# Kernel optimization log

Hardware: AMD Instinct MI355X
Metric: run time of the kernel (lower is better)

Reference implementation:

```python
import jax, jax.numpy as jnp
import numpy as np

SHIFT = 7  # shift_size; pad = 3


def _gn(x, w, b, eps=1e-5):
    # GroupNorm(1, C): normalize over (C,H,W) per sample, affine per channel
    m = jnp.mean(x, axis=(1, 2, 3), keepdims=True)
    v = jnp.var(x, axis=(1, 2, 3), keepdims=True)
    return (x - m) * jax.lax.rsqrt(v + eps) * w[None, :, None, None] + b[None, :, None, None]


def _conv1x1(x, w, b):
    return jnp.einsum('bchw,oc->bohw', x, w) + b[None, :, None, None]


def _gelu(x):
    return jax.nn.gelu(x, approximate=False)


def _shift_h(x, size):
    # CUDA kernel semantics: g = c // ceil(C/size); s = -(g - size//2);
    # out[n,c,h,w] = x[n,c,h+s,w] if in-bounds else 0  (dim=2)
    B, C, H, W = x.shape
    pad = size // 2
    group = -(-C // size)  # ceil
    s = pad - (jnp.arange(C) // group)              # [C], values in [-pad, pad]
    xp = jnp.pad(x, ((0, 0), (0, 0), (pad, pad), (0, 0)))
    idx = jnp.arange(H)[None, :] + s[:, None] + pad  # [C,H], in [0, H+2p-1]
    c = jnp.arange(C)[:, None]
    return xp[:, c, idx, :]


def _shift_w(x, size):
    return _shift_h(x.swapaxes(2, 3), size).swapaxes(2, 3)


def _axial_shift(x, c1w, c1b, n1w, n1b, c21w, c21b, c22w, c22b, n2w, n2b, c3w, c3b):
    x = _gelu(_gn(_conv1x1(x, c1w, c1b), n1w, n1b))
    x_lr = _shift_w(x, SHIFT)
    x_td = _shift_h(x, SHIFT)
    x_lr = _gelu(_conv1x1(x_lr, c21w, c21b))
    x_td = _gelu(_conv1x1(x_td, c22w, c22b))
    x = _gn(x_lr + x_td, n2w, n2b)
    return _conv1x1(x, c3w, c3b)


def setup_inputs() -> dict:
    B, C, H, W = 16, 256, 56, 56
    HID = 4 * C
    key = jax.random.key(0)
    ks = jax.random.split(key, 8)
    wscale = 0.05
    inp = {
        'x': jax.random.normal(ks[0], (B, C, H, W), jnp.float32),
        'n1_w': jnp.ones((C,), jnp.float32), 'n1_b': jnp.zeros((C,), jnp.float32),
        'as_c1_w': jax.random.normal(ks[1], (C, C), jnp.float32) * wscale,
        'as_c1_b': jnp.zeros((C,), jnp.float32),
        'as_n1_w': jnp.ones((C,), jnp.float32), 'as_n1_b': jnp.zeros((C,), jnp.float32),
        'as_c21_w': jax.random.normal(ks[2], (C, C), jnp.float32) * wscale,
        'as_c21_b': jnp.zeros((C,), jnp.float32),
        'as_c22_w': jax.random.normal(ks[3], (C, C), jnp.float32) * wscale,
        'as_c22_b': jnp.zeros((C,), jnp.float32),
        'as_n2_w': jnp.ones((C,), jnp.float32), 'as_n2_b': jnp.zeros((C,), jnp.float32),
        'as_c3_w': jax.random.normal(ks[4], (C, C), jnp.float32) * wscale,
        'as_c3_b': jnp.zeros((C,), jnp.float32),
        'n2_w': jnp.ones((C,), jnp.float32), 'n2_b': jnp.zeros((C,), jnp.float32),
        'fc1_w': jax.random.normal(ks[5], (HID, C), jnp.float32) * wscale,
        'fc1_b': jnp.zeros((HID,), jnp.float32),
        'fc2_w': jax.random.normal(ks[6], (C, HID), jnp.float32) * wscale,
        'fc2_b': jnp.zeros((C,), jnp.float32),
    }
    return inp


def reference(x, n1_w, n1_b, as_c1_w, as_c1_b, as_n1_w, as_n1_b,
              as_c21_w, as_c21_b, as_c22_w, as_c22_b, as_n2_w, as_n2_b,
              as_c3_w, as_c3_b, n2_w, n2_b, fc1_w, fc1_b, fc2_w, fc2_b):
    # AxialShiftedBlock: x = x + AxialShift(norm1(x)); x = x + Mlp(norm2(x))
    h = _gn(x, n1_w, n1_b)
    h = _axial_shift(h, as_c1_w, as_c1_b, as_n1_w, as_n1_b,
                     as_c21_w, as_c21_b, as_c22_w, as_c22_b,
                     as_n2_w, as_n2_b, as_c3_w, as_c3_b)
    x = x + h
    h = _gn(x, n2_w, n2_b)
    h = _gelu(_conv1x1(h, fc1_w, fc1_b))
    h = _conv1x1(h, fc2_w, fc2_b)
    return x + h
```

## Files before the change

### kernel.cpp

```cpp
#include <hip/hip_runtime.h>

typedef __attribute__((ext_vector_type(4))) float f32x4;
typedef __attribute__((ext_vector_type(8))) short bf16x8;
typedef __attribute__((ext_vector_type(4))) unsigned short u16x4;
typedef unsigned short u16;

#define HW 3136
#define NSEG 49
#define NELF 802816.0f
#define EPS 1e-5f

__device__ __forceinline__ short f2bf(float f) {
  union { float f; unsigned u; } v; v.f = f;
  unsigned r = (v.u + 0x7FFFu + ((v.u >> 16) & 1u)) >> 16;
  return (short)r;
}
__device__ __forceinline__ float b2f(u16 u) {
  union { unsigned u; float f; } v; v.u = ((unsigned)u) << 16;
  return v.f;
}
__device__ __forceinline__ float fgelu(float x) {
  float x2 = x * x;
  float u = x * (0.7978845608f + 0.0356774081f * x2);
  float e = __expf(-2.0f * u);
  return x * __builtin_amdgcn_rcpf(1.0f + e);
}
__device__ __forceinline__ void gload16(const void* g, void* l) {
  __builtin_amdgcn_global_load_lds(
      (const __attribute__((address_space(1))) void*)(uintptr_t)g,
      (__attribute__((address_space(3))) void*)(unsigned)(uintptr_t)l,
      16, 0, 0);
}

__global__ void wfold_kernel(const float* __restrict__ c1, const float* __restrict__ c21,
                             const float* __restrict__ c22, const float* __restrict__ c3,
                             const float* __restrict__ fc1, const float* __restrict__ fc2,
                             const float* __restrict__ n1w, const float* __restrict__ an2w,
                             const float* __restrict__ n2w, u16* __restrict__ out) {
  int i = (blockIdx.x * 256 + threadIdx.x) * 4;
  const float* src; int off; const float* scale = nullptr;
  if (i < 65536)       { src = c1;  off = 0;       scale = n1w; }
  else if (i < 131072) { src = c21; off = 65536; }
  else if (i < 196608) { src = c22; off = 131072; }
  else if (i < 262144) { src = c3;  off = 196608;  scale = an2w; }
  else if (i < 524288) { src = fc1; off = 262144;  scale = n2w; }
  else                 { src = fc2; off = 524288; }
  int li = i - off;
  float4 v = *(const float4*)(src + li);
  if (scale) {
    float4 g = *(const float4*)(scale + (li & 255));
    v.x *= g.x; v.y *= g.y; v.z *= g.z; v.w *= g.w;
  }
  u16x4 o4; o4[0] = (u16)f2bf(v.x); o4[1] = (u16)f2bf(v.y); o4[2] = (u16)f2bf(v.z); o4[3] = (u16)f2bf(v.w);
  *(u16x4*)(out + i) = o4;
}

__global__ void rowsum_kernel(const float* __restrict__ c1w, const float* __restrict__ c1b,
                              const float* __restrict__ n1w, const float* __restrict__ n1b,
                              const float* __restrict__ c3w, const float* __restrict__ c3b,
                              const float* __restrict__ an2w, const float* __restrict__ an2b,
                              const float* __restrict__ fc1w, const float* __restrict__ fc1b,
                              const float* __restrict__ n2w, const float* __restrict__ n2b,
                              float* __restrict__ sums) {
  int o = blockIdx.x * 256 + threadIdx.x;
  const float *W, *gw, *gb, *cb; float *Sg, *Sb; int row;
  if (o < 256)      { W = c1w;  gw = n1w;  gb = n1b;  cb = c1b;  Sg = sums;        Sb = sums + 256;  row = o; }
  else if (o < 512) { W = c3w;  gw = an2w; gb = an2b; cb = c3b;  Sg = sums + 512;  Sb = sums + 768;  row = o - 256; }
  else              { W = fc1w; gw = n2w;  gb = n2b;  cb = fc1b; Sg = sums + 1024; Sb = sums + 2048; row = o - 512; }
  float sg = 0.f, sb = 0.f;
  for (int c = 0; c < 256; c += 4) {
    float4 w = *(const float4*)(W + (size_t)row * 256 + c);
    float4 g = *(const float4*)(gw + c);
    float4 b = *(const float4*)(gb + c);
    sg += w.x * g.x + w.y * g.y + w.z * g.z + w.w * g.w;
    sb += w.x * b.x + w.y * b.y + w.z * b.z + w.w * b.w;
  }
  Sg[row] = sg; Sb[row] = sb + cb[row];
}

__global__ __launch_bounds__(256) void t0_kernel(const float* __restrict__ x,
                                                 u16* __restrict__ xT, float* __restrict__ st) {
  __shared__ __align__(16) u16 tile[64 * 256];
  const int t = threadIdx.x;
  const int n = blockIdx.x / NSEG;
  const int hw0 = (blockIdx.x % NSEG) * 64;
  const int pix = t & 63;
  float s = 0.f, q = 0.f;
#pragma unroll
  for (int r = 0; r < 16; ++r) {
    int cq = (t >> 6) + (r << 2);
    int c = cq * 4;
    u16x4 o4;
#pragma unroll
    for (int i = 0; i < 4; ++i) {
      float v = x[((size_t)n * 256 + c + i) * HW + hw0 + pix];
      s += v; q += v * v;
      o4[i] = (u16)f2bf(v);
    }
    int u = cq ^ ((pix & 15) << 2);
    *(u16x4*)((char*)tile + pix * 512 + u * 8) = o4;
  }
  __syncthreads();
  {
    const int p2 = t >> 2;
#pragma unroll
    for (int r = 0; r < 8; ++r) {
      int oct = (t & 3) + (r << 2);
      int up = (2 * oct) ^ ((p2 & 15) << 2);
      bf16x8 v = *(const bf16x8*)((char*)tile + p2 * 512 + up * 8);
      *(bf16x8*)&xT[((size_t)n * HW + hw0 + p2) * 256 + oct * 8] = v;
    }
  }
  __syncthreads();
  float* red = (float*)tile;
  red[t] = s; red[256 + t] = q;
  __syncthreads();
  for (int off = 128; off > 0; off >>= 1) {
    if (t < off) { red[t] += red[t + off]; red[256 + t] += red[256 + t + off]; }
    __syncthreads();
  }
  if (t == 0) { atomicAdd(&st[n * 2], red[0]); atomicAdd(&st[n * 2 + 1], red[256]); }
}

__global__ void e2_kernel(const u16* __restrict__ y, u16* __restrict__ tb,
                          const float* __restrict__ gw, const float* __restrict__ gb,
                          const float* __restrict__ stats) {
  const size_t NG = (size_t)16 * HW * 32;
  for (size_t g = (size_t)blockIdx.x * blockDim.x + threadIdx.x; g < NG;
       g += (size_t)gridDim.x * blockDim.x) {
    size_t base = g * 8;
    int n = (int)(base / 802816);
    int c0 = (int)(base & 255);
    float sm = stats[n * 2], sq = stats[n * 2 + 1];
    float mn = sm * (1.0f / NELF);
    float rstd = rsqrtf(sq * (1.0f / NELF) - mn * mn + EPS);
    bf16x8 v = *(const bf16x8*)(y + base);
    bf16x8 o;
#pragma unroll
    for (int j = 0; j < 8; ++j) {
      float sc = rstd * gw[c0 + j];
      float sh = gb[c0 + j] - mn * sc;
      o[j] = f2bf(fgelu(b2f((u16)v[j]) * sc + sh));
    }
    *(bf16x8*)(tb + base) = o;
  }
}

template<int PRO, int EPI, int OTOT>
__global__ __launch_bounds__(512, 2) void gemmW(
    const u16* __restrict__ actT, const u16* __restrict__ wt,
    const float* __restrict__ Sg, const float* __restrict__ Sb,
    const float* __restrict__ stats_in, float* __restrict__ stats_out,
    const u16* __restrict__ residCL, u16* __restrict__ outT)
{
  constexpr bool FOLD = (EPI == 0 || EPI == 1 || EPI == 2);
  __shared__ __align__(16) u16 lds[72704];
  const int t = threadIdx.x;
  const int lane = t & 63, wave = t >> 6;
  const int fr = lane & 15, fq = lane >> 4;
  const int wo = wave >> 1, wp = wave & 1;
  const int n = blockIdx.x / 14;
  const int hw0 = (blockIdx.x % 14) * 224;
  const int obase = blockIdx.y << 8;
  const size_t nHW = (size_t)n * HW;

  {
    int u0 = t, u1 = t + 512;
    int r0 = u0 >> 2, sg0 = ((u0 & 3) - (r0 >> 1)) & 3;
    int r1 = u1 >> 2, sg1 = ((u1 & 3) - (r1 >> 1)) & 3;
    const u16* w0 = wt + (size_t)(obase + r0) * 256 + sg0 * 8;
    const u16* w1 = wt + (size_t)(obase + r1) * 256 + sg1 * 8;
#pragma unroll
    for (int k = 0; k < 8; ++k) {
      gload16(w0 + k * 32, &lds[k * 8192 + wave * 512]);
      gload16(w1 + k * 32, &lds[k * 8192 + 4096 + wave * 512]);
    }
  }

  const bool bact = (t < 448);
  const int brow = t >> 1;
  const int bp = hw0 + brow;
  int bwp = 0;
  if (PRO == 1) bwp = bp % 56;
  if (PRO == 2) bwp = bp / 56;
  const int bj0 = (t & 1) * 2;
  const u16* bsrc = actT + (nHW + bp) * 256;

  auto loadBu = [&](int c0, bf16x8& v) {
    if (PRO == 0) {
      v = *(const bf16x8*)(bsrc + c0);
    } else {
      int g0 = c0 / 37;
      int js = (g0 + 1) * 37 - c0;
      int s0 = 3 - g0;
      if (js >= 8) {
        if ((unsigned)(bwp + s0) < 56u) {
          int dp = (PRO == 1) ? s0 : 56 * s0;
          v = *(const bf16x8*)(bsrc + dp * 256 + c0);
        } else {
          v = (bf16x8){0, 0, 0, 0, 0, 0, 0, 0};
        }
      } else {
#pragma unroll
        for (int j = 0; j < 8; ++j) {
          int s = s0 - (j >= js ? 1 : 0);
          int dp = (PRO == 1) ? s : 56 * s;
          int pp = bp + dp; pp = pp < 0 ? 0 : (pp > HW - 1 ? HW - 1 : pp);
          u16 uv = actT[(nHW + pp) * 256 + c0 + j];
          v[j] = ((unsigned)(bwp + s) < 56u) ? (short)uv : (short)0;
        }
      }
    }
  };

  int aU[4], bO[7];
#pragma unroll
  for (int os = 0; os < 4; ++os) { int row = wo * 64 + os * 16 + fr; aU[os] = (4 * row + ((fq + (row >> 1)) & 3)) * 8; }
#pragma unroll
  for (int ps = 0; ps < 7; ++ps) bO[ps] = 65536 + (fq * 224 + wp * 112 + ps * 16 + fr) * 8;

  f32x4 acc[4][7];
#pragma unroll
  for (int a = 0; a < 4; ++a)
#pragma unroll
    for (int b = 0; b < 7; ++b) acc[a][b] = (f32x4){0.f, 0.f, 0.f, 0.f};

  {
    bf16x8 v0, v1;
    if (bact) { loadBu(bj0 * 8, v0); loadBu(bj0 * 8 + 8, v1); }
    asm volatile("s_waitcnt vmcnt(0)" ::: "memory");
    if (bact) {
      *(bf16x8*)&lds[65536 + (bj0 * 224 + brow) * 8] = v0;
      *(bf16x8*)&lds[65536 + ((bj0 + 1) * 224 + brow) * 8] = v1;
    }
  }
  __syncthreads();

#pragma unroll
  for (int k = 0; k < 8; ++k) {
    bf16x8 n0, n1;
    if (k < 7 && bact) { loadBu((k + 1) * 32 + bj0 * 8, n0); loadBu((k + 1) * 32 + bj0 * 8 + 8, n1); }
    bf16x8 afr[4], bfr[7];
#pragma unroll
    for (int os = 0; os < 4; ++os) afr[os] = *(const bf16x8*)&lds[k * 8192 + aU[os]];
#pragma unroll
    for (int ps = 0; ps < 7; ++ps) bfr[ps] = *(const bf16x8*)&lds[bO[ps]];
#pragma unroll
    for (int os = 0; os < 4; ++os)
#pragma unroll
      for (int ps = 0; ps < 7; ++ps)
        acc[os][ps] = __builtin_amdgcn_mfma_f32_16x16x32_bf16(afr[os], bfr[ps], acc[os][ps], 0, 0, 0);
    __builtin_amdgcn_s_barrier();
    if (k < 7) {
      if (bact) {
        *(bf16x8*)&lds[65536 + (bj0 * 224 + brow) * 8] = n0;
        *(bf16x8*)&lds[65536 + ((bj0 + 1) * 224 + brow) * 8] = n1;
      }
      asm volatile("s_waitcnt lgkmcnt(0)" ::: "memory");
      __builtin_amdgcn_sched_barrier(0);
      __builtin_amdgcn_s_barrier();
    }
  }
  __syncthreads();

  char* tl = (char*)lds;
  float mr = 0.f, rstd = 1.f;
  if (FOLD) {
    float sm = stats_in[n * 2], sq = stats_in[n * 2 + 1];
    float mn = sm * (1.0f / NELF);
    rstd = rsqrtf(sq * (1.0f / NELF) - mn * mn + EPS);
    mr = mn * rstd;
  }
  float lsum = 0.f, lsq = 0.f;
#pragma unroll
  for (int os = 0; os < 4; ++os) {
    const int obl = wo * 64 + os * 16 + fq * 4;
    const int ob = obase + obl;
    float be[4];
    if (FOLD) {
      float4 g4 = *(const float4*)&Sg[ob];
      float4 s4 = *(const float4*)&Sb[ob];
      be[0] = s4.x - mr * g4.x; be[1] = s4.y - mr * g4.y;
      be[2] = s4.z - mr * g4.z; be[3] = s4.w - mr * g4.w;
    } else {
      float4 s4 = *(const float4*)&Sb[obl];
      be[0] = s4.x; be[1] = s4.y; be[2] = s4.z; be[3] = s4.w;
    }
#pragma unroll
    for (int ps = 0; ps < 7; ++ps) {
      const int pix = wp * 112 + ps * 16 + fr;
      u16x4 rv = {0, 0, 0, 0};
      if (EPI == 1 || EPI == 5)
        rv = *(const u16x4*)&residCL[(nHW + hw0 + pix) * 256 + obl];
      u16x4 pk;
#pragma unroll
      for (int j = 0; j < 4; ++j) {
        float v = FOLD ? fmaf(acc[os][ps][j], rstd, be[j]) : (acc[os][ps][j] + be[j]);
        if (EPI == 2 || EPI == 4 || EPI == 5) v = fgelu(v);
        if (EPI == 1 || EPI == 5) v += b2f(rv[j]);
        if (EPI == 0 || EPI == 1 || EPI == 5) { lsum += v; lsq += v * v; }
        pk[j] = (u16)f2bf(v);
      }
      const int qd = wo * 16 + os * 4 + fq;
      const int uq = qd ^ ((pix & 15) << 2);
      *(u16x4*)(tl + pix * 512 + uq * 8) = pk;
    }
  }
  __syncthreads();
#pragma unroll
  for (int r = 0; r < 14; ++r) {
    int idx = t + r * 512;
    int pix = idx >> 5, oct = idx & 31;
    int up = (2 * oct) ^ ((pix & 15) << 2);
    bf16x8 v = *(const bf16x8*)(tl + pix * 512 + up * 8);
    *(bf16x8*)&outT[(nHW + hw0 + pix) * OTOT + obase + oct * 8] = v;
  }

  if (EPI == 0 || EPI == 1 || EPI == 5) {
    __syncthreads();
    float* red = (float*)lds;
    red[t] = lsum; red[512 + t] = lsq;
    __syncthreads();
    for (int off = 256; off > 0; off >>= 1) {
      if (t < off) { red[t] += red[t + off]; red[512 + t] += red[512 + t + off]; }
      __syncthreads();
    }
    if (t == 0) { atomicAdd(&stats_out[n * 2], red[0]); atomicAdd(&stats_out[n * 2 + 1], red[512]); }
  }
}

__global__ __launch_bounds__(512, 2) void gemmF(
    const u16* __restrict__ hidT, const u16* __restrict__ wt,
    const float* __restrict__ bias, const u16* __restrict__ residCL,
    float* __restrict__ out_f32)
{
  __shared__ __align__(16) u16 lds[30720];
  const int t = threadIdx.x;
  const int lane = t & 63, wave = t >> 6;
  const int fr = lane & 15, fq = lane >> 4;
  const int wo = wave >> 1, wp = wave & 1;
  const int n = blockIdx.x / 14;
  const int hw0 = (blockIdx.x % 14) * 224;
  const size_t nHW = (size_t)n * HW;

  int u0 = t, u1 = t + 512;
  int r0 = u0 >> 2, sg0 = ((u0 & 3) - (r0 >> 1)) & 3;
  int r1 = u1 >> 2, sg1 = ((u1 & 3) - (r1 >> 1)) & 3;
  const u16* wA0 = wt + (size_t)r0 * 1024 + sg0 * 8;
  const u16* wA1 = wt + (size_t)r1 * 1024 + sg1 * 8;
  const int c1 = (2 * wave) % 14, c2 = (2 * wave + 1) % 14;
  const int ub1 = c1 * 64 + lane, ub2 = c2 * 64 + lane;
  const u16* hb1 = hidT + (nHW + hw0 + ub1 % 224) * 1024 + (ub1 / 224) * 8;
  const u16* hb2 = hidT + (nHW + hw0 + ub2 % 224) * 1024 + (ub2 / 224) * 8;

  auto stgf = [&](int bs, int k0) {
    gload16(wA0 + k0, &lds[bs * 8192 + wave * 512]);
    gload16(wA1 + k0, &lds[bs * 8192 + 4096 + wave * 512]);
    gload16(hb1 + k0, &lds[16384 + bs * 7168 + c1 * 512]);
    gload16(hb2 + k0, &lds[16384 + bs * 7168 + c2 * 512]);
  };

  int aU[4], bO[7];
#pragma unroll
  for (int os = 0; os < 4; ++os) { int row = wo * 64 + os * 16 + fr; aU[os] = (4 * row + ((fq + (row >> 1)) & 3)) * 8; }
#pragma unroll
  for (int ps = 0; ps < 7; ++ps) bO[ps] = 16384 + (fq * 224 + wp * 112 + ps * 16 + fr) * 8;

  f32x4 acc[4][7];
#pragma unroll
  for (int a = 0; a < 4; ++a)
#pragma unroll
    for (int b = 0; b < 7; ++b) acc[a][b] = (f32x4){0.f, 0.f, 0.f, 0.f};

  stgf(0, 0);
  __syncthreads();
  for (int ks = 0; ks < 32; ++ks) {
    const int bs = ks & 1;
    if (ks < 31) stgf(bs ^ 1, (ks + 1) * 32);
    bf16x8 afr[4], bfr[7];
#pragma unroll
    for (int os = 0; os < 4; ++os) afr[os] = *(const bf16x8*)&lds[bs * 8192 + aU[os]];
#pragma unroll
    for (int ps = 0; ps < 7; ++ps) bfr[ps] = *(const bf16x8*)&lds[bs * 7168 + bO[ps]];
#pragma unroll
    for (int os = 0; os < 4; ++os)
#pragma unroll
      for (int ps = 0; ps < 7; ++ps)
        acc[os][ps] = __builtin_amdgcn_mfma_f32_16x16x32_bf16(afr[os], bfr[ps], acc[os][ps], 0, 0, 0);
    __syncthreads();
  }

#pragma unroll
  for (int os = 0; os < 4; ++os) {
    const int ob = wo * 64 + os * 16 + fq * 4;
    float4 b4 = *(const float4*)&bias[ob];
    float bb[4] = {b4.x, b4.y, b4.z, b4.w};
#pragma unroll
    for (int ps = 0; ps < 7; ++ps) {
      const int pix = wp * 112 + ps * 16 + fr;
      u16x4 rv = *(const u16x4*)&residCL[(nHW + hw0 + pix) * 256 + ob];
#pragma unroll
      for (int j = 0; j < 4; ++j)
        out_f32[((size_t)n * 256 + ob + j) * HW + hw0 + pix] = acc[os][ps][j] + bb[j] + b2f(rv[j]);
    }
  }
}

extern "C" void kernel_launch(void* const* d_in, const int* in_sizes, int n_in,
                              void* d_out, int out_size, void* d_ws, size_t ws_size,
                              hipStream_t stream) {
  const float* x     = (const float*)d_in[0];
  const float* n1_w  = (const float*)d_in[1];
  const float* n1_b  = (const float*)d_in[2];
  const float* c1_w  = (const float*)d_in[3];
  const float* c1_b  = (const float*)d_in[4];
  const float* an1_w = (const float*)d_in[5];
  const float* an1_b = (const float*)d_in[6];
  const float* c21_w = (const float*)d_in[7];
  const float* c21_b = (const float*)d_in[8];
  const float* c22_w = (const float*)d_in[9];
  const float* c22_b = (const float*)d_in[10];
  const float* an2_w = (const float*)d_in[11];
  const float* an2_b = (const float*)d_in[12];
  const float* c3_w  = (const float*)d_in[13];
  const float* c3_b  = (const float*)d_in[14];
  const float* n2_w  = (const float*)d_in[15];
  const float* n2_b  = (const float*)d_in[16];
  const float* fc1_w = (const float*)d_in[17];
  const float* fc1_b = (const float*)d_in[18];
  const float* fc2_w = (const float*)d_in[19];
  const float* fc2_b = (const float*)d_in[20];

  char* ws = (char*)d_ws;
  float* stats = (float*)ws;
  float* sums  = (float*)(ws + 1024);
  u16* wbuf = (u16*)(ws + 16384);
  u16* wb_c1g  = wbuf;
  u16* wb_c21  = wbuf + 65536;
  u16* wb_c22  = wbuf + 131072;
  u16* wb_c3g  = wbuf + 196608;
  u16* wb_fc1g = wbuf + 262144;
  u16* wb_fc2  = wbuf + 524288;
  const size_t AB = 25690112;
  char* A0 = ws + 1638400;
  u16* xT  = (u16*)(A0);
  u16* yT  = (u16*)(A0 + AB);
  u16* tT  = (u16*)(A0 + 2 * AB);
  u16* zA  = (u16*)(A0 + 3 * AB);
  u16* zT  = (u16*)(A0 + AB);
  u16* x2T = (u16*)(A0 + 4 * AB);
  u16* hid = (u16*)(A0);
  float* out = (float*)d_out;

  hipMemsetAsync(stats, 0, 512, stream);
  wfold_kernel<<<768, 256, 0, stream>>>(c1_w, c21_w, c22_w, c3_w, fc1_w, fc2_w,
                                        n1_w, an2_w, n2_w, wbuf);
  rowsum_kernel<<<6, 256, 0, stream>>>(c1_w, c1_b, n1_w, n1_b, c3_w, c3_b, an2_w, an2_b,
                                       fc1_w, fc1_b, n2_w, n2_b, sums);
  t0_kernel<<<784, 256, 0, stream>>>(x, xT, stats + 0);
  gemmW<0, 0, 256><<<dim3(224, 1), 512, 0, stream>>>(
      xT, wb_c1g, sums, sums + 256, stats + 0, stats + 32, nullptr, yT);
  e2_kernel<<<2048, 256, 0, stream>>>(yT, tT, an1_w, an1_b, stats + 32);
  gemmW<1, 4, 256><<<dim3(224, 1), 512, 0, stream>>>(
      tT, wb_c21, nullptr, c21_b, nullptr, nullptr, nullptr, zA);
  gemmW<2, 5, 256><<<dim3(224, 1), 512, 0, stream>>>(
      tT, wb_c22, nullptr, c22_b, nullptr, stats + 64, zA, zT);
  gemmW<0, 1, 256><<<dim3(224, 1), 512, 0, stream>>>(
      zT, wb_c3g, sums + 512, sums + 768, stats + 64, stats + 96, xT, x2T);
  gemmW<0, 2, 1024><<<dim3(224, 4), 512, 0, stream>>>(
      x2T, wb_fc1g, sums + 1024, sums + 2048, stats + 96, nullptr, nullptr, hid);
  gemmF<<<224, 512, 0, stream>>>(hid, wb_fc2, fc2_b, x2T, out);
}
```

Baseline: 289.9 us.

## Fuse dual shift GEMMs and the fc1→fc2 MLP into single kernels

Replaces the two separate shifted 1x1 conv GEMMs with one kernel that gathers both shifted inputs and computes both branches, summing their GELUs in-register. This avoids writing and re-reading the intermediate zA buffer. The fc1 and fc2 GEMMs are fused so the 1024-wide hidden activation stays in LDS chunk by chunk and never round-trips through global memory. The cost is smaller per-block tiles (112 pixels, 32 output rows per wave), more LDS use, and more complex staging, which may reduce MFMA efficiency and occupancy.

Result: no change. 286.2 us (-1.3%).

```diff
diff --git a/kernel.cpp b/kernel.cpp
--- a/kernel.cpp
+++ b/kernel.cpp
@@ -146,195 +146,14 @@
   }
 }
 
-template<int PRO, int EPI, int OTOT>
-__global__ __launch_bounds__(512, 2) void gemmW(
+template<int EPI>
+__global__ __launch_bounds__(512, 2) void gemmW2(
     const u16* __restrict__ actT, const u16* __restrict__ wt,
     const float* __restrict__ Sg, const float* __restrict__ Sb,
     const float* __restrict__ stats_in, float* __restrict__ stats_out,
     const u16* __restrict__ residCL, u16* __restrict__ outT)
 {
-  constexpr bool FOLD = (EPI == 0 || EPI == 1 || EPI == 2);
-  __shared__ __align__(16) u16 lds[72704];
-  const int t = threadIdx.x;
-  const int lane = t & 63, wave = t >> 6;
-  const int fr = lane & 15, fq = lane >> 4;
-  const int wo = wave >> 1, wp = wave & 1;
-  const int n = blockIdx.x / 14;
-  const int hw0 = (blockIdx.x % 14) * 224;
-  const int obase = blockIdx.y << 8;
-  const size_t nHW = (size_t)n * HW;
-
-  {
-    int u0 = t, u1 = t + 512;
-    int r0 = u0 >> 2, sg0 = ((u0 & 3) - (r0 >> 1)) & 3;
-    int r1 = u1 >> 2, sg1 = ((u1 & 3) - (r1 >> 1)) & 3;
-    const u16* w0 = wt + (size_t)(obase + r0) * 256 + sg0 * 8;
-    const u16* w1 = wt + (size_t)(obase + r1) * 256 + sg1 * 8;
-#pragma unroll
-    for (int k = 0; k < 8; ++k) {
-      gload16(w0 + k * 32, &lds[k * 8192 + wave * 512]);
-      gload16(w1 + k * 32, &lds[k * 8192 + 4096 + wave * 512]);
-    }
-  }
-
-  const bool bact = (t < 448);
-  const int brow = t >> 1;
-  const int bp = hw0 + brow;
-  int bwp = 0;
-  if (PRO == 1) bwp = bp % 56;
-  if (PRO == 2) bwp = bp / 56;
-  const int bj0 = (t & 1) * 2;
-  const u16* bsrc = actT + (nHW + bp) * 256;
-
-  auto loadBu = [&](int c0, bf16x8& v) {
-    if (PRO == 0) {
-      v = *(const bf16x8*)(bsrc + c0);
-    } else {
-      int g0 = c0 / 37;
-      int js = (g0 + 1) * 37 - c0;
-      int s0 = 3 - g0;
-      if (js >= 8) {
-        if ((unsigned)(bwp + s0) < 56u) {
-          int dp = (PRO == 1) ? s0 : 56 * s0;
-          v = *(const bf16x8*)(bsrc + dp * 256 + c0);
-        } else {
-          v = (bf16x8){0, 0, 0, 0, 0, 0, 0, 0};
-        }
-      } else {
-#pragma unroll
-        for (int j = 0; j < 8; ++j) {
-          int s = s0 - (j >= js ? 1 : 0);
-          int dp = (PRO == 1) ? s : 56 * s;
-          int pp = bp + dp; pp = pp < 0 ? 0 : (pp > HW - 1 ? HW - 1 : pp);
-          u16 uv = actT[(nHW + pp) * 256 + c0 + j];
-          v[j] = ((unsigned)(bwp + s) < 56u) ? (short)uv : (short)0;
-        }
-      }
-    }
-  };
-
-  int aU[4], bO[7];
-#pragma unroll
-  for (int os = 0; os < 4; ++os) { int row = wo * 64 + os * 16 + fr; aU[os] = (4 * row + ((fq + (row >> 1)) & 3)) * 8; }
-#pragma unroll
-  for (int ps = 0; ps < 7; ++ps) bO[ps] = 65536 + (fq * 224 + wp * 112 + ps * 16 + fr) * 8;
-
-  f32x4 acc[4][7];
-#pragma unroll
-  for (int a = 0; a < 4; ++a)
-#pragma unroll
-    for (int b = 0; b < 7; ++b) acc[a][b] = (f32x4){0.f, 0.f, 0.f, 0.f};
-
-  {
-    bf16x8 v0, v1;
-    if (bact) { loadBu(bj0 * 8, v0); loadBu(bj0 * 8 + 8, v1); }
-    asm volatile("s_waitcnt vmcnt(0)" ::: "memory");
-    if (bact) {
-      *(bf16x8*)&lds[65536 + (bj0 * 224 + brow) * 8] = v0;
-      *(bf16x8*)&lds[65536 + ((bj0 + 1) * 224 + brow) * 8] = v1;
-    }
-  }
-  __syncthreads();
-
-#pragma unroll
-  for (int k = 0; k < 8; ++k) {
-    bf16x8 n0, n1;
-    if (k < 7 && bact) { loadBu((k + 1) * 32 + bj0 * 8, n0); loadBu((k + 1) * 32 + bj0 * 8 + 8, n1); }
-    bf16x8 afr[4], bfr[7];
-#pragma unroll
-    for (int os = 0; os < 4; ++os) afr[os] = *(const bf16x8*)&lds[k * 8192 + aU[os]];
-#pragma unroll
-    for (int ps = 0; ps < 7; ++ps) bfr[ps] = *(const bf16x8*)&lds[bO[ps]];
-#pragma unroll
-    for (int os = 0; os < 4; ++os)
-#pragma unroll
-      for (int ps = 0; ps < 7; ++ps)
-        acc[os][ps] = __builtin_amdgcn_mfma_f32_16x16x32_bf16(afr[os], bfr[ps], acc[os][ps], 0, 0, 0);
-    __builtin_amdgcn_s_barrier();
-    if (k < 7) {
-      if (bact) {
-        *(bf16x8*)&lds[65536 + (bj0 * 224 + brow) * 8] = n0;
-        *(bf16x8*)&lds[65536 + ((bj0 + 1) * 224 + brow) * 8] = n1;
-      }
-      asm volatile("s_waitcnt lgkmcnt(0)" ::: "memory");
-      __builtin_amdgcn_sched_barrier(0);
-      __builtin_amdgcn_s_barrier();
-    }
-  }
-  __syncthreads();
-
-  char* tl = (char*)lds;
-  float mr = 0.f, rstd = 1.f;
-  if (FOLD) {
-    float sm = stats_in[n * 2], sq = stats_in[n * 2 + 1];
-    float mn = sm * (1.0f / NELF);
-    rstd = rsqrtf(sq * (1.0f / NELF) - mn * mn + EPS);
-    mr = mn * rstd;
-  }
-  float lsum = 0.f, lsq = 0.f;
-#pragma unroll
-  for (int os = 0; os < 4; ++os) {
-    const int obl = wo * 64 + os * 16 + fq * 4;
-    const int ob = obase + obl;
-    float be[4];
-    if (FOLD) {
-      float4 g4 = *(const float4*)&Sg[ob];
-      float4 s4 = *(const float4*)&Sb[ob];
-      be[0] = s4.x - mr * g4.x; be[1] = s4.y - mr * g4.y;
-      be[2] = s4.z - mr * g4.z; be[3] = s4.w - mr * g4.w;
-    } else {
-      float4 s4 = *(const float4*)&Sb[obl];
-      be[0] = s4.x; be[1] = s4.y; be[2] = s4.z; be[3] = s4.w;
-    }
-#pragma unroll
-    for (int ps = 0; ps < 7; ++ps) {
-      const int pix = wp * 112 + ps * 16 + fr;
-      u16x4 rv = {0, 0, 0, 0};
-      if (EPI == 1 || EPI == 5)
-        rv = *(const u16x4*)&residCL[(nHW + hw0 + pix) * 256 + obl];
-      u16x4 pk;
-#pragma unroll
-      for (int j = 0; j < 4; ++j) {
-        float v = FOLD ? fmaf(acc[os][ps][j], rstd, be[j]) : (acc[os][ps][j] + be[j]);
-        if (EPI == 2 || EPI == 4 || EPI == 5) v = fgelu(v);
-        if (EPI == 1 || EPI == 5) v += b2f(rv[j]);
-        if (EPI == 0 || EPI == 1 || EPI == 5) { lsum += v; lsq += v * v; }
-        pk[j] = (u16)f2bf(v);
-      }
-      const int qd = wo * 16 + os * 4 + fq;
-      const int uq = qd ^ ((pix & 15) << 2);
-      *(u16x4*)(tl + pix * 512 + uq * 8) = pk;
-    }
-  }
-  __syncthreads();
-#pragma unroll
-  for (int r = 0; r < 14; ++r) {
-    int idx = t + r * 512;
-    int pix = idx >> 5, oct = idx & 31;
-    int up = (2 * oct) ^ ((pix & 15) << 2);
-    bf16x8 v = *(const bf16x8*)(tl + pix * 512 + up * 8);
-    *(bf16x8*)&outT[(nHW + hw0 + pix) * OTOT + obase + oct * 8] = v;
-  }
-
-  if (EPI == 0 || EPI == 1 || EPI == 5) {
-    __syncthreads();
-    float* red = (float*)lds;
-    red[t] = lsum; red[512 + t] = lsq;
-    __syncthreads();
-    for (int off = 256; off > 0; off >>= 1) {
-      if (t < off) { red[t] += red[t + off]; red[512 + t] += red[512 + t + off]; }
-      __syncthreads();
-    }
-    if (t == 0) { atomicAdd(&stats_out[n * 2], red[0]); atomicAdd(&stats_out[n * 2 + 1], red[512]); }
-  }
-}
-
-__global__ __launch_bounds__(512, 2) void gemmF(
-    const u16* __restrict__ hidT, const u16* __restrict__ wt,
-    const float* __restrict__ bias, const u16* __restrict__ residCL,
-    float* __restrict__ out_f32)
-{
-  __shared__ __align__(16) u16 lds[30720];
+  __shared__ __align__(16) u16 lds[79872];
   const int t = threadIdx.x;
   const int lane = t & 63, wave = t >> 6;
   const int fr = lane & 15, fq = lane >> 4;
@@ -343,45 +162,55 @@
   const int hw0 = (blockIdx.x % 14) * 224;
   const size_t nHW = (size_t)n * HW;
 
-  int u0 = t, u1 = t + 512;
-  int r0 = u0 >> 2, sg0 = ((u0 & 3) - (r0 >> 1)) & 3;
-  int r1 = u1 >> 2, sg1 = ((u1 & 3) - (r1 >> 1)) & 3;
-  const u16* wA0 = wt + (size_t)r0 * 1024 + sg0 * 8;
-  const u16* wA1 = wt + (size_t)r1 * 1024 + sg1 * 8;
-  const int c1 = (2 * wave) % 14, c2 = (2 * wave + 1) % 14;
-  const int ub1 = c1 * 64 + lane, ub2 = c2 * 64 + lane;
-  const u16* hb1 = hidT + (nHW + hw0 + ub1 % 224) * 1024 + (ub1 / 224) * 8;
-  const u16* hb2 = hidT + (nHW + hw0 + ub2 % 224) * 1024 + (ub2 / 224) * 8;
-
-  auto stgf = [&](int bs, int k0) {
-    gload16(wA0 + k0, &lds[bs * 8192 + wave * 512]);
-    gload16(wA1 + k0, &lds[bs * 8192 + 4096 + wave * 512]);
-    gload16(hb1 + k0, &lds[16384 + bs * 7168 + c1 * 512]);
-    gload16(hb2 + k0, &lds[16384 + bs * 7168 + c2 * 512]);
+  {
+    int u0 = t, u1 = t + 512;
+    int r0 = u0 >> 2, sg0 = ((u0 & 3) - (r0 >> 1)) & 3;
+    int r1 = u1 >> 2, sg1 = ((u1 & 3) - (r1 >> 1)) & 3;
+    const u16* w0 = wt + (size_t)r0 * 256 + sg0 * 8;
+    const u16* w1 = wt + (size_t)r1 * 256 + sg1 * 8;
+#pragma unroll
+    for (int k = 0; k < 8; ++k) {
+      gload16(w0 + k * 32, &lds[k * 8192 + wave * 512]);
+      gload16(w1 + k * 32, &lds[k * 8192 + 4096 + wave * 512]);
+    }
+  }
+
+  int aU[4], bO[7];
+#pragma unroll
+  for (int os = 0; os < 4; ++os) { int row = wo * 64 + os * 16 + fr; aU[os] = (4 * row + ((fq + (row >> 1)) & 3)) * 8; }
+#pragma unroll
+  for (int ps = 0; ps < 7; ++ps) bO[ps] = (fq * 224 + wp * 112 + ps * 16 + fr) * 8;
+
+  auto stageB = [&](int par, int ks) {
+    if (wave < 7) {
+#pragma unroll
+      for (int i = 0; i < 2; ++i) {
+        int ub = wave * 128 + i * 64;
+        int u = ub + lane;
+        int j = u / 224, p = u - j * 224;
+        gload16(actT + (nHW + hw0 + p) * 256 + ks * 32 + j * 8,
+                &lds[65536 + par * 7168 + ub * 8]);
+      }
+    }
   };
 
-  int aU[4], bO[7];
-#pragma unroll
-  for (int os = 0; os < 4; ++os) { int row = wo * 64 + os * 16 + fr; aU[os] = (4 * row + ((fq + (row >> 1)) & 3)) * 8; }
-#pragma unroll
-  for (int ps = 0; ps < 7; ++ps) bO[ps] = 16384 + (fq * 224 + wp * 112 + ps * 16 + fr) * 8;
-
   f32x4 acc[4][7];
 #pragma unroll
   for (int a = 0; a < 4; ++a)
 #pragma unroll
     for (int b = 0; b < 7; ++b) acc[a][b] = (f32x4){0.f, 0.f, 0.f, 0.f};
 
-  stgf(0, 0);
-  __syncthreads();
-  for (int ks = 0; ks < 32; ++ks) {
-    const int bs = ks & 1;
-    if (ks < 31) stgf(bs ^ 1, (ks + 1) * 32);
+  stageB(0, 0);
+  __syncthreads();
+
+#pragma unroll
+  for (int k = 0; k < 8; ++k) {
+    if (k < 7) stageB((k + 1) & 1, k + 1);
     bf16x8 afr[4], bfr[7];
 #pragma unroll
-    for (int os = 0; os < 4; ++os) afr[os] = *(const bf16x8*)&lds[bs * 8192 + aU[os]];
-#pragma unroll
-    for (int ps = 0; ps < 7; ++ps) bfr[ps] = *(const bf16x8*)&lds[bs * 7168 + bO[ps]];
+    for (int os = 0; os < 4; ++os) afr[os] = *(const bf16x8*)&lds[k * 8192 + aU[os]];
+#pragma unroll
+    for (int ps = 0; ps < 7; ++ps) bfr[ps] = *(const bf16x8*)&lds[65536 + (k & 1) * 7168 + bO[ps]];
 #pragma unroll
     for (int os = 0; os < 4; ++os)
 #pragma unroll
@@ -390,18 +219,323 @@
     __syncthreads();
   }
 
+  char* tl = (char*)lds;
+  float sm = stats_in[n * 2], sq = stats_in[n * 2 + 1];
+  float mn = sm * (1.0f / NELF);
+  float rstd = rsqrtf(sq * (1.0f / NELF) - mn * mn + EPS);
+  float mr = mn * rstd;
+  float lsum = 0.f, lsq = 0.f;
 #pragma unroll
   for (int os = 0; os < 4; ++os) {
     const int ob = wo * 64 + os * 16 + fq * 4;
-    float4 b4 = *(const float4*)&bias[ob];
-    float bb[4] = {b4.x, b4.y, b4.z, b4.w};
+    float4 g4 = *(const float4*)&Sg[ob];
+    float4 s4 = *(const float4*)&Sb[ob];
+    float be[4] = {s4.x - mr * g4.x, s4.y - mr * g4.y, s4.z - mr * g4.z, s4.w - mr * g4.w};
 #pragma unroll
     for (int ps = 0; ps < 7; ++ps) {
       const int pix = wp * 112 + ps * 16 + fr;
-      u16x4 rv = *(const u16x4*)&residCL[(nHW + hw0 + pix) * 256 + ob];
-#pragma unroll
-      for (int j = 0; j < 4; ++j)
-        out_f32[((size_t)n * 256 + ob + j) * HW + hw0 + pix] = acc[os][ps][j] + bb[j] + b2f(rv[j]);
+      u16x4 rv = {0, 0, 0, 0};
+      if (EPI == 1) rv = *(const u16x4*)&residCL[(nHW + hw0 + pix) * 256 + ob];
+      u16x4 pk;
+#pragma unroll
+      for (int j = 0; j < 4; ++j) {
+        float v = fmaf(acc[os][ps][j], rstd, be[j]);
+        if (EPI == 1) v += b2f(rv[j]);
+        lsum += v; lsq += v * v;
+        pk[j] = (u16)f2bf(v);
+      }
+      const int qd = wo * 16 + os * 4 + fq;
+      const int uq = qd ^ ((pix & 15) << 2);
+      *(u16x4*)(tl + pix * 512 + uq * 8) = pk;
+    }
+  }
+  __syncthreads();
+#pragma unroll
+  for (int r = 0; r < 14; ++r) {
+    int idx = t + r * 512;
+    int pix = idx >> 5, oct = idx & 31;
+    int up = (2 * oct) ^ ((pix & 15) << 2);
+    bf16x8 v = *(const bf16x8*)(tl + pix * 512 + up * 8);
+    *(bf16x8*)&outT[(nHW + hw0 + pix) * 256 + oct * 8] = v;
+  }
+  __syncthreads();
+  float* red = (float*)lds;
+  red[t] = lsum; red[512 + t] = lsq;
+  __syncthreads();
+  for (int off = 256; off > 0; off >>= 1) {
+    if (t < off) { red[t] += red[t + off]; red[512 + t] += red[512 + t + off]; }
+    __syncthreads();
+  }
+  if (t == 0) { atomicAdd(&stats_out[n * 2], red[0]); atomicAdd(&stats_out[n * 2 + 1], red[512]); }
+}
+
+__global__ __launch_bounds__(512, 2) void gemm_dual4(
+    const u16* __restrict__ tT, const u16* __restrict__ w21, const u16* __restrict__ w22,
+    const float* __restrict__ b21, const float* __restrict__ b22,
+    float* __restrict__ stats_out, u16* __restrict__ zT)
+{
+  __shared__ __align__(16) u16 lds[47616];
+  const int t = threadIdx.x;
+  const int lane = t & 63, wave = t >> 6;
+  const int fr = lane & 15, fq = lane >> 4;
+  const int n = blockIdx.x / 28;
+  const int hw0 = (blockIdx.x % 28) * 112;
+  const size_t nHW = (size_t)n * HW;
+
+  const int u = (t < 448) ? t : 447;
+  const int jl = u / 112, p = u - jl * 112;
+  const int pix = hw0 + p;
+  const int wc = pix % 56, hc = pix / 56;
+
+  bf16x8 gA0, gA1, gB0, gB1;
+  auto gatherIssue = [&](int ks) {
+    int c0 = ks * 32 + jl * 8;
+    int g0 = c0 / 37;
+    int s0 = 3 - g0;
+    int pa0 = pix + s0;           pa0 = pa0 < 0 ? 0 : (pa0 > HW - 1 ? HW - 1 : pa0);
+    int pa1 = pix + s0 - 1;       pa1 = pa1 < 0 ? 0 : (pa1 > HW - 1 ? HW - 1 : pa1);
+    int pb0 = pix + 56 * s0;      pb0 = pb0 < 0 ? 0 : (pb0 > HW - 1 ? HW - 1 : pb0);
+    int pb1 = pix + 56 * (s0 - 1); pb1 = pb1 < 0 ? 0 : (pb1 > HW - 1 ? HW - 1 : pb1);
+    gA0 = *(const bf16x8*)(tT + (nHW + pa0) * 256 + c0);
+    gA1 = *(const bf16x8*)(tT + (nHW + pa1) * 256 + c0);
+    gB0 = *(const bf16x8*)(tT + (nHW + pb0) * 256 + c0);
+    gB1 = *(const bf16x8*)(tT + (nHW + pb1) * 256 + c0);
+  };
+  auto gatherWrite = [&](int par, int ks) {
+    int c0 = ks * 32 + jl * 8;
+    int g0 = c0 / 37;
+    int s0 = 3 - g0;
+    int js = (g0 + 1) * 37 - c0; if (js > 8) js = 8;
+    bool a0 = (unsigned)(wc + s0) < 56u, a1 = (unsigned)(wc + s0 - 1) < 56u;
+    bool b0 = (unsigned)(hc + s0) < 56u, b1 = (unsigned)(hc + s0 - 1) < 56u;
+    bf16x8 va, vb;
+#pragma unroll
+    for (int j = 0; j < 8; ++j) {
+      bool lo = j < js;
+      va[j] = lo ? (a0 ? gA0[j] : (short)0) : (a1 ? gA1[j] : (short)0);
+      vb[j] = lo ? (b0 ? gB0[j] : (short)0) : (b1 ? gB1[j] : (short)0);
+    }
+    if (t < 448) {
+      *(bf16x8*)&lds[32768 + par * 3712 + (jl * 116 + p) * 8] = va;
+      *(bf16x8*)&lds[40192 + par * 3712 + (jl * 116 + p) * 8] = vb;
+    }
+  };
+  auto stageW = [&](int par, int ks) {
+    int u0 = t; int r0 = u0 >> 2, sg0 = ((u0 & 3) - (r0 >> 1)) & 3;
+    int u1 = t + 512; int r1 = u1 >> 2, sg1 = ((u1 & 3) - (r1 >> 1)) & 3;
+    gload16(w21 + (size_t)r0 * 256 + ks * 32 + sg0 * 8, &lds[par * 8192 + wave * 512]);
+    gload16(w21 + (size_t)r1 * 256 + ks * 32 + sg1 * 8, &lds[par * 8192 + 4096 + wave * 512]);
+    gload16(w22 + (size_t)r0 * 256 + ks * 32 + sg0 * 8, &lds[16384 + par * 8192 + wave * 512]);
+    gload16(w22 + (size_t)r1 * 256 + ks * 32 + sg1 * 8, &lds[16384 + par * 8192 + 4096 + wave * 512]);
+  };
+
+  int aU[2], bP[7];
+#pragma unroll
+  for (int os = 0; os < 2; ++os) { int row = wave * 32 + os * 16 + fr; aU[os] = (4 * row + ((fq + (row >> 1)) & 3)) * 8; }
+#pragma unroll
+  for (int ps = 0; ps < 7; ++ps) bP[ps] = (fq * 116 + ps * 16 + fr) * 8;
+
+  f32x4 accA[2][7], accB[2][7];
+#pragma unroll
+  for (int a = 0; a < 2; ++a)
+#pragma unroll
+    for (int b = 0; b < 7; ++b) { accA[a][b] = (f32x4){0, 0, 0, 0}; accB[a][b] = (f32x4){0, 0, 0, 0}; }
+
+  gatherIssue(0);
+  stageW(0, 0);
+  gatherWrite(0, 0);
+  gatherIssue(1);
+  __syncthreads();
+
+#pragma unroll
+  for (int k = 0; k < 8; ++k) {
+    if (k < 7) stageW((k + 1) & 1, k + 1);
+    bf16x8 afA[2], afB[2], bfA[7], bfB[7];
+#pragma unroll
+    for (int os = 0; os < 2; ++os) {
+      afA[os] = *(const bf16x8*)&lds[(k & 1) * 8192 + aU[os]];
+      afB[os] = *(const bf16x8*)&lds[16384 + (k & 1) * 8192 + aU[os]];
+    }
+#pragma unroll
+    for (int ps = 0; ps < 7; ++ps) {
+      bfA[ps] = *(const bf16x8*)&lds[32768 + (k & 1) * 3712 + bP[ps]];
+      bfB[ps] = *(const bf16x8*)&lds[40192 + (k & 1) * 3712 + bP[ps]];
+    }
+#pragma unroll
+    for (int os = 0; os < 2; ++os)
+#pragma unroll
+      for (int ps = 0; ps < 7; ++ps) {
+        accA[os][ps] = __builtin_amdgcn_mfma_f32_16x16x32_bf16(afA[os], bfA[ps], accA[os][ps], 0, 0, 0);
+        accB[os][ps] = __builtin_amdgcn_mfma_f32_16x16x32_bf16(afB[os], bfB[ps], accB[os][ps], 0, 0, 0);
+      }
+    if (k < 7) {
+      gatherWrite((k + 1) & 1, k + 1);
+      if (k < 6) gatherIssue(k + 2);
+    }
+    __syncthreads();
+  }
+
+  char* tl = (char*)lds;
+  float lsum = 0.f, lsq = 0.f;
+#pragma unroll
+  for (int os = 0; os < 2; ++os) {
+    const int ob = wave * 32 + os * 16 + fq * 4;
+    float4 a4 = *(const float4*)&b21[ob];
+    float4 c4 = *(const float4*)&b22[ob];
+#pragma unroll
+    for (int ps = 0; ps < 7; ++ps) {
+      const int pixL = ps * 16 + fr;
+      u16x4 pk;
+      float ba[4] = {a4.x, a4.y, a4.z, a4.w};
+      float bb[4] = {c4.x, c4.y, c4.z, c4.w};
+#pragma unroll
+      for (int j = 0; j < 4; ++j) {
+        float z = fgelu(accA[os][ps][j] + ba[j]) + fgelu(accB[os][ps][j] + bb[j]);
+        lsum += z; lsq += z * z;
+        pk[j] = (u16)f2bf(z);
+      }
+      const int qd = wave * 8 + os * 4 + fq;
+      const int uq = qd ^ ((pixL & 15) << 2);
+      *(u16x4*)(tl + pixL * 512 + uq * 8) = pk;
+    }
+  }
+  __syncthreads();
+#pragma unroll
+  for (int r = 0; r < 7; ++r) {
+    int idx = t + r * 512;
+    int pixL = idx >> 5, oct = idx & 31;
+    int up = (2 * oct) ^ ((pixL & 15) << 2);
+    bf16x8 v = *(const bf16x8*)(tl + pixL * 512 + up * 8);
+    *(bf16x8*)&zT[(nHW + hw0 + pixL) * 256 + oct * 8] = v;
+  }
+  __syncthreads();
+  float* red = (float*)lds;
+  red[t] = lsum; red[512 + t] = lsq;
+  __syncthreads();
+  for (int off = 256; off > 0; off >>= 1) {
+    if (t < off) { red[t] += red[t + off]; red[512 + t] += red[512 + t + off]; }
+    __syncthreads();
+  }
+  if (t == 0) { atomicAdd(&stats_out[n * 2], red[0]); atomicAdd(&stats_out[n * 2 + 1], red[512]); }
+}
+
+__global__ __launch_bounds__(512, 2) void gemm_mlp(
+    const u16* __restrict__ x2T, const u16* __restrict__ wfc1, const u16* __restrict__ wfc2,
+    const float* __restrict__ Sg, const float* __restrict__ Sb, const float* __restrict__ bias2,
+    const float* __restrict__ stats_in, float* __restrict__ out_f32)
+{
+  __shared__ __align__(16) u16 lds[75008];
+  const int t = threadIdx.x;
+  const int lane = t & 63, wave = t >> 6;
+  const int fr = lane & 15, fq = lane >> 4;
+  const int n = blockIdx.x / 28;
+  const int hw0 = (blockIdx.x % 28) * 112;
+  const size_t nHW = (size_t)n * HW;
+
+  auto stageWm = [&](int par, int s) {
+    int chunk = s >> 4, kk = s & 7;
+    int u0 = t; int r0 = u0 >> 2, sg0 = ((u0 & 3) - (r0 >> 1)) & 3;
+    int u1 = t + 512; int r1 = u1 >> 2, sg1 = ((u1 & 3) - (r1 >> 1)) & 3;
+    if (((s >> 3) & 1) == 0) {
+      gload16(wfc1 + (size_t)(chunk * 256 + r0) * 256 + kk * 32 + sg0 * 8, &lds[par * 8192 + wave * 512]);
+      gload16(wfc1 + (size_t)(chunk * 256 + r1) * 256 + kk * 32 + sg1 * 8, &lds[par * 8192 + 4096 + wave * 512]);
+    } else {
+      gload16(wfc2 + (size_t)r0 * 1024 + chunk * 256 + kk * 32 + sg0 * 8, &lds[par * 8192 + wave * 512]);
+      gload16(wfc2 + (size_t)r1 * 1024 + chunk * 256 + kk * 32 + sg1 * 8, &lds[par * 8192 + 4096 + wave * 512]);
+    }
+  };
+
+#pragma unroll
+  for (int i = 0; i < 7; ++i) {
+    int u = wave * 448 + i * 64 + lane;
+    int j = u / 112, p = u - j * 112;
+    bf16x8 v = *(const bf16x8*)(x2T + (nHW + hw0 + p) * 256 + j * 8);
+    *(bf16x8*)&lds[16384 + (j * 113 + p) * 8] = v;
+  }
+  stageWm(0, 0);
+
+  float sm = stats_in[n * 2], sq = stats_in[n * 2 + 1];
+  float mn = sm * (1.0f / NELF);
+  float rstd = rsqrtf(sq * (1.0f / NELF) - mn * mn + EPS);
+  float mr = mn * rstd;
+
+  int aU[2];
+#pragma unroll
+  for (int os = 0; os < 2; ++os) { int row = wave * 32 + os * 16 + fr; aU[os] = (4 * row + ((fq + (row >> 1)) & 3)) * 8; }
+
+  f32x4 hacc[2][7], oacc[2][7];
+#pragma unroll
+  for (int a = 0; a < 2; ++a)
+#pragma unroll
+    for (int b = 0; b < 7; ++b) { hacc[a][b] = (f32x4){0, 0, 0, 0}; oacc[a][b] = (f32x4){0, 0, 0, 0}; }
+
+  __syncthreads();
+
+  for (int s = 0; s < 64; ++s) {
+    if (s < 63) stageWm((s + 1) & 1, s + 1);
+    const int kk = s & 7;
+    const bool bph = (s >> 3) & 1;
+    bf16x8 afr[2], bfr[7];
+#pragma unroll
+    for (int os = 0; os < 2; ++os) afr[os] = *(const bf16x8*)&lds[(s & 1) * 8192 + aU[os]];
+    if (!bph) {
+#pragma unroll
+      for (int ps = 0; ps < 7; ++ps)
+        bfr[ps] = *(const bf16x8*)&lds[16384 + ((kk * 4 + fq) * 113 + ps * 16 + fr) * 8];
+#pragma unroll
+      for (int os = 0; os < 2; ++os)
+#pragma unroll
+        for (int ps = 0; ps < 7; ++ps)
+          hacc[os][ps] = __builtin_amdgcn_mfma_f32_16x16x32_bf16(afr[os], bfr[ps], hacc[os][ps], 0, 0, 0);
+    } else {
+#pragma unroll
+      for (int ps = 0; ps < 7; ++ps)
+        bfr[ps] = *(const bf16x8*)&lds[45312 + ((kk * 4 + fq) * 116 + ps * 16 + fr) * 8];
+#pragma unroll
+      for (int os = 0; os < 2; ++os)
+#pragma unroll
+        for (int ps = 0; ps < 7; ++ps)
+          oacc[os][ps] = __builtin_amdgcn_mfma_f32_16x16x32_bf16(afr[os], bfr[ps], oacc[os][ps], 0, 0, 0);
+    }
+    if ((s & 15) == 7) {
+      const int hcb = (s >> 4) * 256;
+#pragma unroll
+      for (int os = 0; os < 2; ++os) {
+        const int hcl = wave * 32 + os * 16 + fq * 4;
+        const int hc = hcb + hcl;
+        float4 g4 = *(const float4*)&Sg[hc];
+        float4 s4 = *(const float4*)&Sb[hc];
+        float be[4] = {s4.x - mr * g4.x, s4.y - mr * g4.y, s4.z - mr * g4.z, s4.w - mr * g4.w};
+        const int jH = hcl >> 3;
+#pragma unroll
+        for (int ps = 0; ps < 7; ++ps) {
+          const int pixL = ps * 16 + fr;
+          u16x4 pk;
+#pragma unroll
+          for (int j = 0; j < 4; ++j)
+            pk[j] = (u16)f2bf(fgelu(fmaf(hacc[os][ps][j], rstd, be[j])));
+          *(u16x4*)&lds[45312 + (jH * 116 + pixL) * 8 + (fq & 1) * 4] = pk;
+          hacc[os][ps] = (f32x4){0, 0, 0, 0};
+        }
+      }
+    }
+    __syncthreads();
+  }
+
+#pragma unroll
+  for (int os = 0; os < 2; ++os) {
+    const int ob = wave * 32 + os * 16 + fq * 4;
+    float4 b4 = *(const float4*)&bias2[ob];
+    float bb[4] = {b4.x, b4.y, b4.z, b4.w};
+#pragma unroll
+    for (int ps = 0; ps < 7; ++ps) {
+      const int pixL = ps * 16 + fr;
+      u16x4 rv = *(const u16x4*)&lds[16384 + ((ob >> 3) * 113 + pixL) * 8 + (ob & 4)];
+#pragma unroll
+      for (int j = 0; j < 4; ++j) {
+        float v = oacc[os][ps][j] + bb[j] + b2f(rv[j]);
+        out_f32[((size_t)n * 256 + ob + j) * HW + hw0 + pixL] = v;
+      }
     }
   }
 }
@@ -446,10 +580,8 @@
   u16* xT  = (u16*)(A0);
   u16* yT  = (u16*)(A0 + AB);
   u16* tT  = (u16*)(A0 + 2 * AB);
-  u16* zA  = (u16*)(A0 + 3 * AB);
-  u16* zT  = (u16*)(A0 + AB);
+  u16* zT  = (u16*)(A0 + 3 * AB);
   u16* x2T = (u16*)(A0 + 4 * AB);
-  u16* hid = (u16*)(A0);
   float* out = (float*)d_out;
 
   hipMemsetAsync(stats, 0, 512, stream);
@@ -458,16 +590,12 @@
   rowsum_kernel<<<6, 256, 0, stream>>>(c1_w, c1_b, n1_w, n1_b, c3_w, c3_b, an2_w, an2_b,
                                        fc1_w, fc1_b, n2_w, n2_b, sums);
   t0_kernel<<<784, 256, 0, stream>>>(x, xT, stats + 0);
-  gemmW<0, 0, 256><<<dim3(224, 1), 512, 0, stream>>>(
-      xT, wb_c1g, sums, sums + 256, stats + 0, stats + 32, nullptr, yT);
+  gemmW2<0><<<224, 512, 0, stream>>>(xT, wb_c1g, sums, sums + 256,
+                                     stats + 0, stats + 32, nullptr, yT);
   e2_kernel<<<2048, 256, 0, stream>>>(yT, tT, an1_w, an1_b, stats + 32);
-  gemmW<1, 4, 256><<<dim3(224, 1), 512, 0, stream>>>(
-      tT, wb_c21, nullptr, c21_b, nullptr, nullptr, nullptr, zA);
-  gemmW<2, 5, 256><<<dim3(224, 1), 512, 0, stream>>>(
-      tT, wb_c22, nullptr, c22_b, nullptr, stats + 64, zA, zT);
-  gemmW<0, 1, 256><<<dim3(224, 1), 512, 0, stream>>>(
-      zT, wb_c3g, sums + 512, sums + 768, stats + 64, stats + 96, xT, x2T);
-  gemmW<0, 2, 1024><<<dim3(224, 4), 512, 0, stream>>>(
-      x2T, wb_fc1g, sums + 1024, sums + 2048, stats + 96, nullptr, nullptr, hid);
-  gemmF<<<224, 512, 0, stream>>>(hid, wb_fc2, fc2_b, x2T, out);
-}
+  gemm_dual4<<<448, 512, 0, stream>>>(tT, wb_c21, wb_c22, c21_b, c22_b, stats + 64, zT);
+  gemmW2<1><<<224, 512, 0, stream>>>(zT, wb_c3g, sums + 512, sums + 768,
+                                     stats + 64, stats + 96, xT, x2T);
+  gemm_mlp<<<448, 512, 0, stream>>>(x2T, wb_fc1g, wb_fc2, sums + 1024, sums + 2048,
+                                    fc2_b, stats + 96, out);
+}
```
